# Kernel tuning notes

Measured on AMD Instinct MI355X. Metric: run time of the kernel, lower is better.

## Reference

```python
import jax, jax.numpy as jnp
import numpy as np

B, NQ, NV = 4, 16384, 16384
DIM, FRAMES = 64, 4
D = DIM * FRAMES            # embed_dims = 256
HEADS, POINTS, LEVELS = 8, 4, 1
HD = D // HEADS             # head_dim = 32
HL, WL = 128, 128           # single-level feature map, HL*WL == NV
EPS = 1e-6


def setup_inputs() -> dict:
    key = jax.random.key(0)
    ks = jax.random.split(key, 14)
    inp = {
        "query": jax.random.normal(ks[0], (B, NQ, D), jnp.float32),
        "feat": jax.random.normal(ks[1], (B, NV, D), jnp.float32),
        "reference_points": jax.random.uniform(ks[2], (B, NQ, LEVELS, 2), jnp.float32),
        "spatial_shapes": jnp.array([[HL, WL]], jnp.int32),
        "level_start_index": jnp.array([0], jnp.int32),
        # LayerNorm params
        "qn_scale": jnp.ones((D,), jnp.float32),
        "qn_bias": jnp.zeros((D,), jnp.float32),
        "fn_scale": jnp.ones((D,), jnp.float32),
        "fn_bias": jnp.zeros((D,), jnp.float32),
        # MSDeformAttn projections
        "W_value": jax.random.normal(ks[3], (D, D), jnp.float32) / np.sqrt(D),
        "b_value": jnp.zeros((D,), jnp.float32),
        "W_off": jax.random.normal(ks[4], (D, HEADS * LEVELS * POINTS * 2), jnp.float32) * 0.01,
        "b_off": jax.random.normal(ks[5], (HEADS * LEVELS * POINTS * 2,), jnp.float32) * 0.5,
        "W_attn": jax.random.normal(ks[6], (D, HEADS * LEVELS * POINTS), jnp.float32) * 0.02,
        "b_attn": jnp.zeros((HEADS * LEVELS * POINTS,), jnp.float32),
        "W_out": jax.random.normal(ks[7], (D, D), jnp.float32) / np.sqrt(D),
        "b_out": jnp.zeros((D,), jnp.float32),
        # gamma is a learned scale (init 0 in the module; randomized here so it contributes)
        "gamma": jax.random.normal(ks[8], (D,), jnp.float32) * 0.1,
    }
    return inp


def _layer_norm(x, scale, bias):
    mu = jnp.mean(x, axis=-1, keepdims=True)
    var = jnp.mean(jnp.square(x - mu), axis=-1, keepdims=True)
    return (x - mu) * jax.lax.rsqrt(var + EPS) * scale + bias


def _bilinear_gather(v, loc, Hl, Wl):
    # v:   [B, H, N, hd] flattened level values (row-major HxW)
    # loc: [B, H, NQ, P, 2] normalized sampling locations in [0,1]
    # grid_sample semantics: align_corners=False, zero padding
    x = loc[..., 0] * Wl - 0.5
    y = loc[..., 1] * Hl - 0.5
    x0 = jnp.floor(x); y0 = jnp.floor(y)
    x1 = x0 + 1.0;     y1 = y0 + 1.0
    wx1 = x - x0; wx0 = 1.0 - wx1
    wy1 = y - y0; wy0 = 1.0 - wy1
    out = 0.0
    for xi, yi, w in ((x0, y0, wx0 * wy0), (x1, y0, wx1 * wy0),
                      (x0, y1, wx0 * wy1), (x1, y1, wx1 * wy1)):
        inb = (xi >= 0) & (xi < Wl) & (yi >= 0) & (yi < Hl)
        idx = (jnp.clip(yi, 0, Hl - 1) * Wl + jnp.clip(xi, 0, Wl - 1)).astype(jnp.int32)
        Bc, Hc, NQc, Pc = idx.shape
        g = jnp.take_along_axis(v, idx.reshape(Bc, Hc, NQc * Pc)[..., None], axis=2)
        g = g.reshape(Bc, Hc, NQc, Pc, -1)          # [B, H, NQ, P, hd]
        out = out + g * (w * inb)[..., None]
    return out


def reference(query, feat, reference_points, spatial_shapes, level_start_index,
              qn_scale, qn_bias, fn_scale, fn_bias,
              W_value, b_value, W_off, b_off, W_attn, b_attn, W_out, b_out, gamma):
    Bq, nq, _ = query.shape
    q = _layer_norm(query, qn_scale, qn_bias)
    v = _layer_norm(feat, fn_scale, fn_bias)

    # value projection -> per-head values [B, H, NV, hd]
    value = (v @ W_value + b_value).reshape(Bq, -1, HEADS, HD).transpose(0, 2, 1, 3)

    # sampling offsets [B, NQ, H, L, P, 2] and attention weights (softmax over L*P)
    off = (q @ W_off + b_off).reshape(Bq, nq, HEADS, LEVELS, POINTS, 2)
    aw = jax.nn.softmax((q @ W_attn + b_attn).reshape(Bq, nq, HEADS, LEVELS * POINTS), axis=-1)
    aw = aw.reshape(Bq, nq, HEADS, LEVELS, POINTS)

    ss = np.asarray(spatial_shapes)          # static level geometry
    lsi = np.asarray(level_start_index)
    offset_norm = ss[:, ::-1].astype(np.float32)  # (W, H) per level
    # sampling locations [B, NQ, H, L, P, 2]
    loc = reference_points[:, :, None, :, None, :] + off / offset_norm[None, None, None, :, None, :]

    acc = jnp.zeros((Bq, HEADS, nq, HD), query.dtype)
    for l in range(LEVELS):
        Hl, Wl = int(ss[l, 0]), int(ss[l, 1])
        start = int(lsi[l])
        v_l = value[:, :, start:start + Hl * Wl]                # [B, H, Hl*Wl, hd]
        loc_l = loc[:, :, :, l].transpose(0, 2, 1, 3, 4)        # [B, H, NQ, P, 2]
        sampled = _bilinear_gather(v_l, loc_l, Hl, Wl)          # [B, H, NQ, P, hd]
        aw_l = aw[:, :, :, l].transpose(0, 2, 1, 3)             # [B, H, NQ, P]
        acc = acc + jnp.einsum('bhnpd,bhnp->bhnd', sampled, aw_l)

    out = acc.transpose(0, 2, 1, 3).reshape(Bq, nq, D) @ W_out + b_out
    return query + gamma * out
```

## Files before the change

### kernel.cpp

```cpp
#include <hip/hip_runtime.h>

#define NQ 16384
#define NV 16384
#define DMODEL 256
#define SAMPN (4 * 16384 * 8)
#define VPLANE 65536

typedef __bf16 bf16x8 __attribute__((ext_vector_type(8)));
typedef float f32x4 __attribute__((ext_vector_type(4)));

__device__ __forceinline__ unsigned short f2bf(float x) {
    union { float f; unsigned int u; } v; v.f = x;
    unsigned int r = v.u + 0x7fff + ((v.u >> 16) & 1);
    return (unsigned short)(r >> 16);
}
__device__ __forceinline__ float blo(unsigned int u) {
    union { unsigned int u; float f; } v; v.u = u << 16; return v.f;
}
__device__ __forceinline__ float bhi(unsigned int u) {
    union { unsigned int u; float f; } v; v.u = u & 0xFFFF0000u; return v.f;
}
__device__ __forceinline__ f32x4 mfma16(bf16x8 a, bf16x8 b, f32x4 c) {
    return __builtin_amdgcn_mfma_f32_16x16x32_bf16(a, b, c, 0, 0, 0);
}

__global__ __launch_bounds__(256) void k_prep(
    const float* __restrict__ Wv, const float* __restrict__ Woff,
    const float* __restrict__ Wattn, const float* __restrict__ Wout,
    const float* __restrict__ fns, const float* __restrict__ fnb,
    const float* __restrict__ qns, const float* __restrict__ qnb,
    const float* __restrict__ b_value, const float* __restrict__ b_off,
    const float* __restrict__ b_attn,
    unsigned short* __restrict__ WtV, unsigned short* __restrict__ WtC,
    unsigned short* __restrict__ WtO,
    float* __restrict__ csumV, float* __restrict__ preV,
    float* __restrict__ csumC, float* __restrict__ preC) {
    const int blk = blockIdx.x;
    if (blk < 608) {
        int t = blk * 256 + threadIdx.x;
        if (t < 65536) { int n = t >> 8, k = t & 255; WtV[t] = f2bf(fns[k] * Wv[k * 256 + n]); return; }
        t -= 65536;
        if (t < 65536) { int n = t >> 8, k = t & 255; WtO[t] = f2bf(Wout[k * 256 + n]); return; }
        t -= 65536;
        if (t < 24576) {
            int j = t >> 8, k = t & 255;
            float w = (j < 64) ? Woff[k * 64 + j] : Wattn[k * 32 + (j - 64)];
            WtC[j * 256 + k] = f2bf(qns[k] * w);
        }
        return;
    }
    if (blk < 612) {
        __shared__ float sCS[4][64], sPR[4][64];
        const int nl = threadIdx.x & 63;
        const int n = (blk - 608) * 64 + nl;
        const int kp = threadIdx.x >> 6;
        float cs = 0.f, pr = 0.f;
        for (int k = kp * 64; k < kp * 64 + 64; ++k) {
            float w = Wv[k * 256 + n];
            cs += fns[k] * w;
            pr += fnb[k] * w;
        }
        sCS[kp][nl] = cs; sPR[kp][nl] = pr;
        __syncthreads();
        if (threadIdx.x < 64) {
            int nn = (blk - 608) * 64 + threadIdx.x;
            csumV[nn] = sCS[0][threadIdx.x] + sCS[1][threadIdx.x] + sCS[2][threadIdx.x] + sCS[3][threadIdx.x];
            preV[nn] = sPR[0][threadIdx.x] + sPR[1][threadIdx.x] + sPR[2][threadIdx.x] + sPR[3][threadIdx.x]
                       + b_value[nn];
        }
        return;
    }
    {
        __shared__ float sCS[2][96], sPR[2][96];
        const int t = threadIdx.x;
        if (t < 192) {
            const int n = t % 96;
            const int kp = t / 96;
            float cs = 0.f, pr = 0.f;
            for (int k = kp * 128; k < kp * 128 + 128; ++k) {
                float w = (n < 64) ? Woff[k * 64 + n] : Wattn[k * 32 + (n - 64)];
                cs += qns[k] * w;
                pr += qnb[k] * w;
            }
            sCS[kp][n] = cs; sPR[kp][n] = pr;
        }
        __syncthreads();
        if (t < 96) {
            csumC[t] = sCS[0][t] + sCS[1][t];
            preC[t] = sPR[0][t] + sPR[1][t] + ((t < 64) ? b_off[t] : b_attn[t - 64]);
        }
        return;
    }
}

#define STAGE_LNSTATS64(srcptr)                                                       \
    {                                                                                 \
        const int t = threadIdx.x;                                                    \
        const float4* src4 = (const float4*)((srcptr) + (size_t)m0 * 256);            \
        _Pragma("unroll 8") for (int i = 0; i < 16; ++i) {                            \
            float4 x = src4[i * 256 + t];                                             \
            const int row = i * 4 + (t >> 6);                                         \
            uint2 pk;                                                                 \
            pk.x = (unsigned)f2bf(x.x) | ((unsigned)f2bf(x.y) << 16);                 \
            pk.y = (unsigned)f2bf(x.z) | ((unsigned)f2bf(x.w) << 16);                 \
            *(uint2*)&A[row * 264 + (t & 63) * 4] = pk;                               \
        }                                                                             \
    }                                                                                 \
    __syncthreads();                                                                  \
    {                                                                                 \
        const int t = threadIdx.x;                                                    \
        const int r = t >> 2, h = t & 3;                                              \
        float s = 0.f, sq = 0.f;                                                      \
        _Pragma("unroll") for (int j = 0; j < 8; ++j) {                               \
            uint4 u = *(const uint4*)&A[r * 264 + h * 64 + j * 8];                    \
            float v0 = blo(u.x), v1 = bhi(u.x), v2 = blo(u.y), v3 = bhi(u.y);         \
            float v4 = blo(u.z), v5 = bhi(u.z), v6 = blo(u.w), v7 = bhi(u.w);         \
            s += v0 + v1 + v2 + v3 + v4 + v5 + v6 + v7;                               \
            sq += v0 * v0 + v1 * v1 + v2 * v2 + v3 * v3 +                             \
                  v4 * v4 + v5 * v5 + v6 * v6 + v7 * v7;                              \
        }                                                                             \
        s += __shfl_xor(s, 1);  sq += __shfl_xor(sq, 1);                              \
        s += __shfl_xor(s, 2);  sq += __shfl_xor(sq, 2);                              \
        if (h == 0) {                                                                 \
            float mu = s * 0.00390625f;                                               \
            muL[r] = mu;                                                              \
            rsL[r] = rsqrtf(sq * 0.00390625f - mu * mu + 1e-6f);                      \
        }                                                                             \
    }

#define MFMA_STEP4(bf, kk)                                                            \
    _Pragma("unroll") for (int m = 0; m < 4; ++m) {                                   \
        bf16x8 a = *(const bf16x8*)&A[(m * 16 + lrow) * 264 + (kk) * 32 + lk];        \
        _Pragma("unroll") for (int i = 0; i < 4; ++i)                                 \
            acc[i][m] = mfma16(bf[i], a, acc[i][m]);                                  \
    }

__global__ __launch_bounds__(256, 4) void k_mlp(
    const float* __restrict__ feat, const float* __restrict__ csumV,
    const float* __restrict__ preV, const unsigned short* __restrict__ WtV,
    unsigned short* __restrict__ value,
    const float* __restrict__ query, const float* __restrict__ refpt,
    const float* __restrict__ csumC, const float* __restrict__ preC,
    const unsigned short* __restrict__ WtC, float4* __restrict__ samples) {
    __shared__ unsigned short A[64 * 264];
    __shared__ float muL[64], rsL[64];
    const int blk = blockIdx.x;
    const int m0 = (blk >> 1) * 64;
    const int lane = threadIdx.x & 63;
    const int w = threadIdx.x >> 6;

    if ((blk & 1) == 0) {
        STAGE_LNSTATS64(feat)
        const int lrow = lane & 15, lk = (lane >> 4) * 8;
        f32x4 acc[4][4];
#pragma unroll
        for (int i = 0; i < 4; ++i)
#pragma unroll
            for (int m = 0; m < 4; ++m) acc[i][m] = (f32x4){0.f, 0.f, 0.f, 0.f};
#define LOADB_V(dst, kk)                                                              \
    _Pragma("unroll") for (int i = 0; i < 4; ++i) dst[i] =                            \
        *(const bf16x8*)(WtV + (size_t)((w * 4 + i) * 16 + lrow) * 256 + (kk) * 32 + lk);
        {
            bf16x8 b0[4], b1[4];
            LOADB_V(b0, 0)
#pragma unroll
            for (int k2 = 0; k2 < 4; ++k2) {
                LOADB_V(b1, k2 * 2 + 1)
                MFMA_STEP4(b0, k2 * 2)
                if (k2 < 3) { LOADB_V(b0, k2 * 2 + 2) }
                MFMA_STEP4(b1, k2 * 2 + 1)
            }
        }
        __syncthreads();
        const int g = lane >> 4;
#pragma unroll
        for (int i = 0; i < 4; ++i) {
            const int col0 = (w * 4 + i) * 16 + g * 4;
            float4 cs = *(const float4*)(csumV + col0);
            float4 pr = *(const float4*)(preV + col0);
#pragma unroll
            for (int m = 0; m < 4; ++m) {
                const int rl = m * 16 + (lane & 15);
                float mu = muL[rl], rs = rsL[rl];
                uint2 r;
                r.x = (unsigned)f2bf(rs * (acc[i][m][0] - mu * cs.x) + pr.x) |
                      ((unsigned)f2bf(rs * (acc[i][m][1] - mu * cs.y) + pr.y) << 16);
                r.y = (unsigned)f2bf(rs * (acc[i][m][2] - mu * cs.z) + pr.z) |
                      ((unsigned)f2bf(rs * (acc[i][m][3] - mu * cs.w) + pr.w) << 16);
                *(uint2*)&A[rl * 264 + col0] = r;
            }
        }
        __syncthreads();
        {
            const int pix = threadIdx.x >> 2;
            const int chunk = threadIdx.x & 3;
#pragma unroll
            for (int h = 0; h < 8; ++h) {
                *(uint4*)(value + ((size_t)h * VPLANE + (m0 + pix)) * 32 + chunk * 8) =
                    *(uint4*)&A[pix * 264 + h * 32 + chunk * 8];
            }
        }
    } else {
        float* DlA = (float*)A;
        const int lrow = lane & 15, g = lane >> 4, lk = g * 8;
        const float4* qrow = (const float4*)(query + (size_t)(m0 + w * 16 + lrow) * 256) + g * 2;
        f32x4 acc[6];
#pragma unroll
        for (int i = 0; i < 6; ++i) acc[i] = (f32x4){0.f, 0.f, 0.f, 0.f};
        float s = 0.f, sq = 0.f;
#pragma unroll
        for (int kk = 0; kk < 8; ++kk) {
            float4 xa = qrow[kk * 8];
            float4 xb = qrow[kk * 8 + 1];
            s  += xa.x + xa.y + xa.z + xa.w + xb.x + xb.y + xb.z + xb.w;
            sq += xa.x * xa.x + xa.y * xa.y + xa.z * xa.z + xa.w * xa.w +
                  xb.x * xb.x + xb.y * xb.y + xb.z * xb.z + xb.w * xb.w;
            union { bf16x8 v; unsigned short u[8]; } af;
            af.u[0] = f2bf(xa.x); af.u[1] = f2bf(xa.y); af.u[2] = f2bf(xa.z); af.u[3] = f2bf(xa.w);
            af.u[4] = f2bf(xb.x); af.u[5] = f2bf(xb.y); af.u[6] = f2bf(xb.z); af.u[7] = f2bf(xb.w);
            bf16x8 b[6];
#pragma unroll
            for (int i = 0; i < 6; ++i)
                b[i] = *(const bf16x8*)(WtC + (size_t)(i * 16 + lrow) * 256 + kk * 32 + lk);
#pragma unroll
            for (int i = 0; i < 6; ++i) acc[i] = mfma16(b[i], af.v, acc[i]);
        }
        s += __shfl_xor(s, 16); sq += __shfl_xor(sq, 16);
        s += __shfl_xor(s, 32); sq += __shfl_xor(sq, 32);
        if (lane < 16) {
            float mu = s * 0.00390625f;
            muL[w * 16 + lane] = mu;
            rsL[w * 16 + lane] = rsqrtf(sq * 0.00390625f - mu * mu + 1e-6f);
        }
        float* Dl = DlA + w * 1600;
#pragma unroll
        for (int i = 0; i < 6; ++i) {
            *(float4*)&Dl[lrow * 100 + i * 16 + g * 4] =
                make_float4(acc[i][0], acc[i][1], acc[i][2], acc[i][3]);
        }
        __syncthreads();
#pragma unroll
        for (int it = 0; it < 2; ++it) {
            int idx = it * 64 + lane;
            int rl = idx >> 3;
            int h = idx & 7;
            int row = m0 + w * 16 + rl;
            float mu = muL[w * 16 + rl], rs = rsL[w * 16 + rl];
            float rx = refpt[(size_t)row * 2 + 0] * 128.f - 0.5f;
            float ry = refpt[(size_t)row * 2 + 1] * 128.f - 0.5f;
            float l0 = rs * (Dl[rl * 100 + 64 + h * 4 + 0] - mu * csumC[64 + h * 4 + 0]) + preC[64 + h * 4 + 0];
            float l1 = rs * (Dl[rl * 100 + 64 + h * 4 + 1] - mu * csumC[64 + h * 4 + 1]) + preC[64 + h * 4 + 1];
            float l2 = rs * (Dl[rl * 100 + 64 + h * 4 + 2] - mu * csumC[64 + h * 4 + 2]) + preC[64 + h * 4 + 2];
            float l3 = rs * (Dl[rl * 100 + 64 + h * 4 + 3] - mu * csumC[64 + h * 4 + 3]) + preC[64 + h * 4 + 3];
            float mx = fmaxf(fmaxf(l0, l1), fmaxf(l2, l3));
            float e0 = __expf(l0 - mx), e1 = __expf(l1 - mx);
            float e2 = __expf(l2 - mx), e3 = __expf(l3 - mx);
            float inv = 1.f / (e0 + e1 + e2 + e3);
            float ww[4] = {e0 * inv, e1 * inv, e2 * inv, e3 * inv};
            size_t trow = (size_t)row * 8 + h;
#pragma unroll
            for (int p = 0; p < 4; ++p) {
                float ox = rs * (Dl[rl * 100 + h * 8 + p * 2 + 0] - mu * csumC[h * 8 + p * 2 + 0]) + preC[h * 8 + p * 2 + 0];
                float oy = rs * (Dl[rl * 100 + h * 8 + p * 2 + 1] - mu * csumC[h * 8 + p * 2 + 1]) + preC[h * 8 + p * 2 + 1];
                samples[(size_t)p * SAMPN + trow] = make_float4(rx + ox, ry + oy, ww[p], 0.f);
            }
        }
    }
}

__global__ __launch_bounds__(256, 4) void k_gatherout(
    const unsigned short* __restrict__ value, const float4* __restrict__ samples,
    const unsigned short* __restrict__ WtO, const float* __restrict__ b_out,
    const float* __restrict__ gamma, const float* __restrict__ query,
    float* __restrict__ out) {
    __shared__ unsigned short A[64 * 264];
    const int m0 = blockIdx.x * 64;
    const int b = m0 >> 14;
    {
        const int t = threadIdx.x;
        const int h = (t >> 2) & 7;
        const int sub = t & 3;
        const unsigned short* vb = value + ((size_t)h * VPLANE + ((size_t)b << 14)) * 32 + sub * 8;
#pragma unroll
        for (int k = 0; k < 8; ++k) {
            const int rl = k * 8 + (t >> 5);
            const size_t trow = (size_t)(m0 + rl) * 8 + h;
            float a0 = 0.f, a1 = 0.f, a2 = 0.f, a3 = 0.f;
            float a4 = 0.f, a5 = 0.f, a6 = 0.f, a7 = 0.f;
#pragma unroll
            for (int p = 0; p < 4; ++p) {
                float4 s = samples[(size_t)p * SAMPN + trow];
                float xf = floorf(s.x), yf = floorf(s.y);
                float fx = s.x - xf, fy = s.y - yf;
                int x0 = (int)xf, y0 = (int)yf;
                int x1 = x0 + 1, y1 = y0 + 1;
                float wgt = s.z;
                bool bx0 = (unsigned)x0 < 128u, bx1 = (unsigned)x1 < 128u;
                bool by0 = (unsigned)y0 < 128u, by1 = (unsigned)y1 < 128u;
                float wt[4];
                wt[0] = (bx0 && by0) ? (1.f - fx) * (1.f - fy) * wgt : 0.f;
                wt[1] = (bx1 && by0) ? fx * (1.f - fy) * wgt : 0.f;
                wt[2] = (bx0 && by1) ? (1.f - fx) * fy * wgt : 0.f;
                wt[3] = (bx1 && by1) ? fx * fy * wgt : 0.f;
                int xc0 = min(max(x0, 0), 127), xc1 = min(max(x1, 0), 127);
                int yc0 = min(max(y0, 0), 127), yc1 = min(max(y1, 0), 127);
                int pix[4];
                pix[0] = yc0 * 128 + xc0; pix[1] = yc0 * 128 + xc1;
                pix[2] = yc1 * 128 + xc0; pix[3] = yc1 * 128 + xc1;
#pragma unroll
                for (int tp = 0; tp < 4; ++tp) {
                    uint4 u = *(const uint4*)(vb + (size_t)pix[tp] * 32);
                    float wq = wt[tp];
                    a0 = fmaf(wq, blo(u.x), a0); a1 = fmaf(wq, bhi(u.x), a1);
                    a2 = fmaf(wq, blo(u.y), a2); a3 = fmaf(wq, bhi(u.y), a3);
                    a4 = fmaf(wq, blo(u.z), a4); a5 = fmaf(wq, bhi(u.z), a5);
                    a6 = fmaf(wq, blo(u.w), a6); a7 = fmaf(wq, bhi(u.w), a7);
                }
            }
            uint4 r;
            r.x = (unsigned)f2bf(a0) | ((unsigned)f2bf(a1) << 16);
            r.y = (unsigned)f2bf(a2) | ((unsigned)f2bf(a3) << 16);
            r.z = (unsigned)f2bf(a4) | ((unsigned)f2bf(a5) << 16);
            r.w = (unsigned)f2bf(a6) | ((unsigned)f2bf(a7) << 16);
            *(uint4*)&A[rl * 264 + h * 32 + sub * 8] = r;
        }
    }
    __syncthreads();
    const int lane = threadIdx.x & 63;
    const int w = threadIdx.x >> 6;
    const int lrow = lane & 15, lk = (lane >> 4) * 8;
    f32x4 acc[4][4];
#pragma unroll
    for (int i = 0; i < 4; ++i)
#pragma unroll
        for (int m = 0; m < 4; ++m) acc[i][m] = (f32x4){0.f, 0.f, 0.f, 0.f};
#define LOADB_O(dst, kk)                                                              \
    _Pragma("unroll") for (int i = 0; i < 4; ++i) dst[i] =                            \
        *(const bf16x8*)(WtO + (size_t)((w * 4 + i) * 16 + lrow) * 256 + (kk) * 32 + lk);
    {
        bf16x8 b0[4], b1[4];
        LOADB_O(b0, 0)
#pragma unroll
        for (int k2 = 0; k2 < 4; ++k2) {
            LOADB_O(b1, k2 * 2 + 1)
            MFMA_STEP4(b0, k2 * 2)
            if (k2 < 3) { LOADB_O(b0, k2 * 2 + 2) }
            MFMA_STEP4(b1, k2 * 2 + 1)
        }
    }
    const int g = lane >> 4;
    float4 bo[4], gm[4];
#pragma unroll
    for (int i = 0; i < 4; ++i) {
        bo[i] = *(const float4*)(b_out + (w * 4 + i) * 16 + g * 4);
        gm[i] = *(const float4*)(gamma + (w * 4 + i) * 16 + g * 4);
    }
#pragma unroll
    for (int m = 0; m < 4; ++m) {
        const size_t row = (size_t)(m0 + m * 16 + (lane & 15));
#pragma unroll
        for (int i = 0; i < 4; ++i) {
            const int col0 = (w * 4 + i) * 16 + g * 4;
            float4 q = *(const float4*)(query + row * 256 + col0);
            float4 o;
            o.x = q.x + gm[i].x * (acc[i][m][0] + bo[i].x);
            o.y = q.y + gm[i].y * (acc[i][m][1] + bo[i].y);
            o.z = q.z + gm[i].z * (acc[i][m][2] + bo[i].z);
            o.w = q.w + gm[i].w * (acc[i][m][3] + bo[i].w);
            *(float4*)(out + row * 256 + col0) = o;
        }
    }
}

extern "C" void kernel_launch(void* const* d_in, const int* in_sizes, int n_in,
                              void* d_out, int out_size, void* d_ws, size_t ws_size,
                              hipStream_t stream) {
    const float* query    = (const float*)d_in[0];
    const float* feat     = (const float*)d_in[1];
    const float* refpt    = (const float*)d_in[2];
    const float* qn_scale = (const float*)d_in[5];
    const float* qn_bias  = (const float*)d_in[6];
    const float* fn_scale = (const float*)d_in[7];
    const float* fn_bias  = (const float*)d_in[8];
    const float* W_value  = (const float*)d_in[9];
    const float* b_value  = (const float*)d_in[10];
    const float* W_off    = (const float*)d_in[11];
    const float* b_off    = (const float*)d_in[12];
    const float* W_attn   = (const float*)d_in[13];
    const float* b_attn   = (const float*)d_in[14];
    const float* W_out    = (const float*)d_in[15];
    const float* b_out    = (const float*)d_in[16];
    const float* gamma    = (const float*)d_in[17];
    float* out = (float*)d_out;

    char* ws = (char*)d_ws;
    unsigned short* WtV   = (unsigned short*)(ws);
    unsigned short* WtO   = (unsigned short*)(ws + 131072);
    unsigned short* WtC   = (unsigned short*)(ws + 262144);
    float* csumV = (float*)(ws + 311296);
    float* preV  = (float*)(ws + 312320);
    float* csumC = (float*)(ws + 313344);
    float* preC  = (float*)(ws + 313856);
    unsigned short* value = (unsigned short*)(ws + 315392);
    float4* samples       = (float4*)(ws + 315392 + 33554432);

    hipLaunchKernelGGL(k_prep, dim3(613), dim3(256), 0, stream,
                       W_value, W_off, W_attn, W_out,
                       fn_scale, fn_bias, qn_scale, qn_bias,
                       b_value, b_off, b_attn,
                       WtV, WtC, WtO, csumV, preV, csumC, preC);
    hipLaunchKernelGGL(k_mlp, dim3(2048), dim3(256), 0, stream,
                       feat, csumV, preV, WtV, value,
                       query, refpt, csumC, preC, WtC, samples);
    hipLaunchKernelGGL(k_gatherout, dim3(1024), dim3(256), 0, stream,
                       value, samples, WtO, b_out, gamma, query, out);
}
```

Baseline: 167.8 us.

## Bucket queries by reference-point tile to improve gather locality

Adds histogram, scan and permutation kernels that sort queries into 8x8 spatial buckets per batch by reference point. The gather/output kernel then processes queries in this permuted order, so each block samples nearby value rows and cache reuse should improve. The cost is three extra small launches, a memset, atomics and indirect reads and writes of query and output rows, which are now scattered. Atomic slot assignment also makes the order within a bucket nondeterministic.

```diff
diff --git a/kernel.cpp b/kernel.cpp
--- a/kernel.cpp
+++ b/kernel.cpp
@@ -91,6 +91,50 @@
         }
         return;
     }
+}
+
+__global__ __launch_bounds__(256) void k_hist(
+    const float* __restrict__ refpt, int* __restrict__ hist) {
+    const int q = blockIdx.x * 256 + threadIdx.x;
+    const int b = q >> 14;
+    float rx = refpt[(size_t)q * 2 + 0], ry = refpt[(size_t)q * 2 + 1];
+    int px = min(max((int)(rx * 128.f), 0), 127);
+    int py = min(max((int)(ry * 128.f), 0), 127);
+    int bucket = (b << 8) | ((py >> 3) << 4) | (px >> 3);
+    atomicAdd(&hist[bucket], 1);
+}
+
+__global__ __launch_bounds__(256) void k_scan(
+    const int* __restrict__ hist, int* __restrict__ base, int* __restrict__ cursor) {
+    __shared__ int tmp[256];
+    const int t = threadIdx.x;
+    int4 h4 = ((const int4*)hist)[t];
+    int tsum = h4.x + h4.y + h4.z + h4.w;
+    tmp[t] = tsum;
+    __syncthreads();
+    for (int d = 1; d < 256; d <<= 1) {
+        int v = (t >= d) ? tmp[t - d] : 0;
+        __syncthreads();
+        tmp[t] += v;
+        __syncthreads();
+    }
+    int excl = tmp[t] - tsum;
+    int4 b4;
+    b4.x = excl; b4.y = excl + h4.x; b4.z = b4.y + h4.y; b4.w = b4.z + h4.z;
+    ((int4*)base)[t] = b4;
+    ((int4*)cursor)[t] = b4;
+}
+
+__global__ __launch_bounds__(256) void k_perm(
+    const float* __restrict__ refpt, int* __restrict__ cursor, int* __restrict__ perm) {
+    const int q = blockIdx.x * 256 + threadIdx.x;
+    const int b = q >> 14;
+    float rx = refpt[(size_t)q * 2 + 0], ry = refpt[(size_t)q * 2 + 1];
+    int px = min(max((int)(rx * 128.f), 0), 127);
+    int py = min(max((int)(ry * 128.f), 0), 127);
+    int bucket = (b << 8) | ((py >> 3) << 4) | (px >> 3);
+    int slot = atomicAdd(&cursor[bucket], 1);
+    perm[slot] = q;
 }
 
 #define STAGE_LNSTATS64(srcptr)                                                       \
@@ -270,21 +314,27 @@
 
 __global__ __launch_bounds__(256, 4) void k_gatherout(
     const unsigned short* __restrict__ value, const float4* __restrict__ samples,
+    const int* __restrict__ perm,
     const unsigned short* __restrict__ WtO, const float* __restrict__ b_out,
     const float* __restrict__ gamma, const float* __restrict__ query,
     float* __restrict__ out) {
     __shared__ unsigned short A[64 * 264];
+    __shared__ int permL[64];
     const int m0 = blockIdx.x * 64;
-    const int b = m0 >> 14;
+    if (threadIdx.x < 64) permL[threadIdx.x] = perm[m0 + threadIdx.x];
+    __syncthreads();
     {
         const int t = threadIdx.x;
         const int h = (t >> 2) & 7;
         const int sub = t & 3;
-        const unsigned short* vb = value + ((size_t)h * VPLANE + ((size_t)b << 14)) * 32 + sub * 8;
 #pragma unroll
         for (int k = 0; k < 8; ++k) {
             const int rl = k * 8 + (t >> 5);
-            const size_t trow = (size_t)(m0 + rl) * 8 + h;
+            const int qp = permL[rl];
+            const int bq = qp >> 14;
+            const unsigned short* vb =
+                value + ((size_t)h * VPLANE + ((size_t)bq << 14)) * 32 + sub * 8;
+            const size_t trow = (size_t)qp * 8 + h;
             float a0 = 0.f, a1 = 0.f, a2 = 0.f, a3 = 0.f;
             float a4 = 0.f, a5 = 0.f, a6 = 0.f, a7 = 0.f;
 #pragma unroll
@@ -357,7 +407,7 @@
     }
 #pragma unroll
     for (int m = 0; m < 4; ++m) {
-        const size_t row = (size_t)(m0 + m * 16 + (lane & 15));
+        const size_t row = (size_t)permL[m * 16 + (lane & 15)];
 #pragma unroll
         for (int i = 0; i < 4; ++i) {
             const int col0 = (w * 4 + i) * 16 + g * 4;
@@ -401,17 +451,25 @@
     float* preV  = (float*)(ws + 312320);
     float* csumC = (float*)(ws + 313344);
     float* preC  = (float*)(ws + 313856);
-    unsigned short* value = (unsigned short*)(ws + 315392);
-    float4* samples       = (float4*)(ws + 315392 + 33554432);
-
+    int* hist    = (int*)(ws + 314368);
+    int* basep   = (int*)(ws + 318464);
+    int* cursor  = (int*)(ws + 322560);
+    int* perm    = (int*)(ws + 326656);
+    unsigned short* value = (unsigned short*)(ws + 655360);
+    float4* samples       = (float4*)(ws + 655360 + 33554432);
+
+    hipMemsetAsync(ws + 314368, 0, 12288, stream);
     hipLaunchKernelGGL(k_prep, dim3(613), dim3(256), 0, stream,
                        W_value, W_off, W_attn, W_out,
                        fn_scale, fn_bias, qn_scale, qn_bias,
                        b_value, b_off, b_attn,
                        WtV, WtC, WtO, csumV, preV, csumC, preC);
+    hipLaunchKernelGGL(k_hist, dim3(256), dim3(256), 0, stream, refpt, hist);
+    hipLaunchKernelGGL(k_scan, dim3(1), dim3(256), 0, stream, hist, basep, cursor);
+    hipLaunchKernelGGL(k_perm, dim3(256), dim3(256), 0, stream, refpt, cursor, perm);
     hipLaunchKernelGGL(k_mlp, dim3(2048), dim3(256), 0, stream,
                        feat, csumV, preV, WtV, value,
                        query, refpt, csumC, preC, WtC, samples);
     hipLaunchKernelGGL(k_gatherout, dim3(1024), dim3(256), 0, stream,
-                       value, samples, WtO, b_out, gamma, query, out);
-}
+                       value, samples, perm, WtO, b_out, gamma, query, out);
+}
```

Result: slower. 177.3 us (+5.6%).
